# Optimization experiments

Measured on AMD Instinct MI355X. Metric: run time of the kernel, lower is better.

The kernel has to match this reference:

```python
import jax, jax.numpy as jnp
import numpy as np

B, C, H, W = 4, 64, 96, 96
O = 64          # out_channel
K = 9           # 3x3 kernel positions
PAD = 1


def conv3x3(x, w, b):
    # NCHW 3x3 conv, stride 1, pad 1
    y = jax.lax.conv_general_dilated(
        x, w, window_strides=(1, 1), padding=((PAD, PAD), (PAD, PAD)),
        dimension_numbers=("NCHW", "OIHW", "NCHW"))
    return y + b[None, :, None, None]


def deform_conv3x3(x, offset, w, b):
    """torchvision-style DeformConv2d, 3x3, stride 1, pad 1, 1 offset group.
    x: [B, Cin, H, W]; offset: [B, 2*K, H, W] ordered (dy, dx) per kernel pos.
    """
    Bb, Cin, Hh, Ww = x.shape
    off = offset.reshape(Bb, K, 2, Hh, Ww)
    ky, kx = jnp.meshgrid(jnp.arange(3), jnp.arange(3), indexing="ij")
    ky = ky.reshape(K).astype(x.dtype)
    kx = kx.reshape(K).astype(x.dtype)
    hh = jnp.arange(Hh, dtype=x.dtype)
    ww = jnp.arange(Ww, dtype=x.dtype)
    # sampling coords: p0 + p_k + delta_p  -> [B, K, H, W]
    py = hh[None, None, :, None] - PAD + ky[None, :, None, None] + off[:, :, 0]
    px = ww[None, None, None, :] - PAD + kx[None, :, None, None] + off[:, :, 1]

    y0 = jnp.floor(py).astype(jnp.int32)
    x0 = jnp.floor(px).astype(jnp.int32)
    dy = py - y0.astype(x.dtype)
    dx = px - x0.astype(x.dtype)

    x_flat = x.reshape(Bb, Cin, Hh * Ww)

    def gather(yi, xi, wgt):
        valid = ((yi >= 0) & (yi < Hh) & (xi >= 0) & (xi < Ww)).astype(x.dtype)
        idx = (jnp.clip(yi, 0, Hh - 1) * Ww + jnp.clip(xi, 0, Ww - 1)).reshape(Bb, -1)
        vals = jax.vmap(lambda xf, ix: xf[:, ix])(x_flat, idx)  # [B, Cin, K*H*W]
        return vals * (wgt * valid).reshape(Bb, 1, -1)

    sampled = (gather(y0,     x0,     (1 - dy) * (1 - dx))
             + gather(y0,     x0 + 1, (1 - dy) * dx)
             + gather(y0 + 1, x0,     dy * (1 - dx))
             + gather(y0 + 1, x0 + 1, dy * dx))
    sampled = sampled.reshape(Bb, Cin, K, Hh, Ww)
    out = jnp.einsum("bckhw,ock->bohw", sampled, w.reshape(O, Cin, K))
    return out + b[None, :, None, None]


def setup_inputs() -> dict:
    key = jax.random.key(0)
    ks = jax.random.split(key, 6)
    ref_feat = jax.random.normal(ks[0], (B, C, H, W), dtype=jnp.float32)
    dist_feat = jax.random.normal(ks[1], (B, C, H, W), dtype=jnp.float32)
    offset_w = jax.random.normal(ks[2], (2 * K, C, 3, 3), dtype=jnp.float32) * 0.01
    offset_b = jnp.zeros((2 * K,), dtype=jnp.float32)
    deform_w = jax.random.normal(ks[3], (O, 3 * C, 3, 3), dtype=jnp.float32) * 0.05
    deform_b = jax.random.normal(ks[4], (O,), dtype=jnp.float32) * 0.05
    return {"ref_feat": ref_feat, "dist_feat": dist_feat,
            "offset_w": offset_w, "offset_b": offset_b,
            "deform_w": deform_w, "deform_b": deform_b}


def reference(ref_feat, dist_feat, offset_w, offset_b, deform_w, deform_b):
    offset = conv3x3(ref_feat, offset_w, offset_b)
    diff = (ref_feat - dist_feat) ** 2
    feat_in = jnp.concatenate((ref_feat, dist_feat, diff), axis=1)  # [B, 3C, H, W]
    feat = deform_conv3x3(feat_in, offset, deform_w, deform_b)
    feat = jax.nn.relu(feat)
    return (feat, diff)
```

## Files before the change

### kernel.cpp

```cpp
#include <hip/hip_runtime.h>
#include <hip/hip_fp16.h>

#define Wd    96
#define Hd    96
#define HW    9216
#define Bn    4
#define Cn    64
#define C3    192
#define On    64
#define NPIX  (Bn*HW)
#define NFEAT (Bn*Cn*HW)
#define NWTB  (9*6*4*512)
#define NWTB2 (18*2*64*8)
#define NRB3  (Bn*(HW/32))

#define HR2   6
#define HC    21
#define HPITCH 400
#define NPR2  (HR2*HC)
#define SELEM (NPR2*24)
#define HALO_B (NPR2*HPITCH)
#define NFBLK 1152

typedef __attribute__((ext_vector_type(8))) short s8v;
typedef __attribute__((ext_vector_type(8))) _Float16 h8v;
typedef __attribute__((ext_vector_type(4))) unsigned int u4v;
typedef __attribute__((ext_vector_type(4))) float f4v;

__device__ __forceinline__ unsigned packh(float lo, float hi) {
    __half2 h = __floats2half2_rn(lo, hi);
    return __builtin_bit_cast(unsigned, h);
}

__global__ __launch_bounds__(256) void repack_wts_kernel(
        const float* __restrict__ ref,
        const float* __restrict__ dist,
        unsigned int* __restrict__ packed,
        float* __restrict__ out_diff,
        const float* __restrict__ dw,
        const float* __restrict__ ow,
        __half* __restrict__ wtb,
        __half* __restrict__ wtb2) {
    __shared__ unsigned lds[96][33];

    int tid = threadIdx.x;

    if (blockIdx.x >= NRB3) {
        int e = (int)(blockIdx.x - NRB3) * 256 + tid;
        if (e < NWTB) {
            int j = e & 7;
            int L = (e >> 3) & 63;
            int mt = (e >> 9) & 3;
            int rest = e >> 11;
            int kc = rest % 6;
            int tap = rest / 6;
            int o = mt * 16 + (L & 15);
            int c = kc * 32 + (L >> 4) * 8 + j;
            wtb[e] = __float2half(dw[((size_t)o * C3 + c) * 9 + tap]);
        } else if (e < NWTB + NWTB2) {
            int e2 = e - NWTB;
            int j = e2 & 7;
            int L = (e2 >> 3) & 63;
            int mt = (e2 >> 9) & 1;
            int kc2 = e2 >> 10;
            int v = mt * 16 + (L & 15);
            int k = kc2 * 32 + ((L >> 4) & 3) * 8 + j;
            int c = k & 63;
            int tap = k >> 6;
            float val = (v < 18) ? ow[((size_t)v * Cn + c) * 9 + tap] : 0.f;
            wtb2[e2] = __float2half(val);
        }
        return;
    }

    int blk = blockIdx.x;
    int b = blk / (HW / 32);
    int pb = (blk - b * (HW / 32)) * 32;
    int pxg = tid & 7;
    int chp = tid >> 3;

    size_t base0 = ((size_t)(b * Cn + 2 * chp)) * HW + pb + pxg * 4;
    size_t base1 = base0 + HW;

    f4v r0 = *(const f4v*)(ref + base0);
    f4v r1 = *(const f4v*)(ref + base1);
    f4v d0 = *(const f4v*)(dist + base0);
    f4v d1 = *(const f4v*)(dist + base1);

    f4v q0 = (r0 - d0) * (r0 - d0);
    f4v q1 = (r1 - d1) * (r1 - d1);
    *(f4v*)(out_diff + base0) = q0;
    *(f4v*)(out_diff + base1) = q1;

#pragma unroll
    for (int j = 0; j < 4; ++j) {
        int p = pxg * 4 + j;
        lds[chp][p]      = packh(r0[j], r1[j]);
        lds[32 + chp][p] = packh(d0[j], d1[j]);
        lds[64 + chp][p] = packh(q0[j], q1[j]);
    }
    __syncthreads();

    {
        int p = tid >> 3;
        int part = tid & 7;
        unsigned* pko = packed + ((size_t)(b * HW + pb) + p) * 96 + part * 12;
#pragma unroll
        for (int q = 0; q < 3; ++q) {
            u4v w;
#pragma unroll
            for (int j = 0; j < 4; ++j)
                w[j] = lds[part * 12 + q * 4 + j][p];
            *(u4v*)(pko + q * 4) = w;
        }
    }
}

struct Ctx {
    int o00, o01, o10, o11;
    int l00, l01, l10, l11;
    float W00, W01, W10, W11;
    int inh;
};

__device__ __forceinline__ Ctx mkctx(int t, int y, int x, int xb, int yb,
                                     float2 o2) {
    Ctx c;
    float py = (float)(y - 1 + t / 3) + o2.x;
    float pxs = (float)(x - 1 + t % 3) + o2.y;
    float fy = floorf(py), fx = floorf(pxs);
    int y0 = (int)fy, x0 = (int)fx;
    int y1 = y0 + 1, x1 = x0 + 1;
    float ay = py - fy, ax = pxs - fx;
    bool vy0 = (unsigned)y0 < (unsigned)Hd;
    bool vy1 = (unsigned)y1 < (unsigned)Hd;
    bool vx0 = (unsigned)x0 < (unsigned)Wd;
    bool vx1 = (unsigned)x1 < (unsigned)Wd;
    c.W00 = (vy0 && vx0) ? (1.f - ay) * (1.f - ax) : 0.f;
    c.W01 = (vy0 && vx1) ? (1.f - ay) * ax : 0.f;
    c.W10 = (vy1 && vx0) ? ay * (1.f - ax) : 0.f;
    c.W11 = (vy1 && vx1) ? ay * ax : 0.f;
    int y0c = min(max(y0, 0), Hd - 1), y1c = min(max(y1, 0), Hd - 1);
    int x0c = min(max(x0, 0), Wd - 1), x1c = min(max(x1, 0), Wd - 1);
    c.o00 = (y0c * Wd + x0c) * (C3 * 2);
    c.o01 = (y0c * Wd + x1c) * (C3 * 2);
    c.o10 = (y1c * Wd + x0c) * (C3 * 2);
    c.o11 = (y1c * Wd + x1c) * (C3 * 2);
    int iy0 = y0c - yb + 2, iy1 = y1c - yb + 2;
    int ix0 = x0c - xb + 3, ix1 = x1c - xb + 3;
    c.inh = ((unsigned)iy0 < (unsigned)HR2) & ((unsigned)iy1 < (unsigned)HR2) &
            ((unsigned)ix0 < (unsigned)HC) & ((unsigned)ix1 < (unsigned)HC);
    c.l00 = (iy0 * HC + ix0) * HPITCH;
    c.l01 = (iy0 * HC + ix1) * HPITCH;
    c.l10 = (iy1 * HC + ix0) * HPITCH;
    c.l11 = (iy1 * HC + ix1) * HPITCH;
    return c;
}

__device__ __forceinline__ __half2 uh2(unsigned u) {
    return __builtin_bit_cast(__half2, u);
}

__device__ __forceinline__ void bilin_mfma(const s8v* rw, const Ctx& cc,
        const s8v* __restrict__ Ap, int t, int kb, int L, f4v* acc) {
    __half2 w00 = __float2half2_rn(cc.W00);
    __half2 w01 = __float2half2_rn(cc.W01);
    __half2 w10 = __float2half2_rn(cc.W10);
    __half2 w11 = __float2half2_rn(cc.W11);
#pragma unroll
    for (int i = 0; i < 3; ++i) {
        int kc = kb + i;
        u4v u00 = __builtin_bit_cast(u4v, rw[0 * 3 + i]);
        u4v u01 = __builtin_bit_cast(u4v, rw[1 * 3 + i]);
        u4v u10 = __builtin_bit_cast(u4v, rw[2 * 3 + i]);
        u4v u11 = __builtin_bit_cast(u4v, rw[3 * 3 + i]);
        u4v bu;
#pragma unroll
        for (int p = 0; p < 4; ++p) {
            __half2 v = __hmul2(uh2(u00[p]), w00);
            v = __hfma2(uh2(u01[p]), w01, v);
            v = __hfma2(uh2(u10[p]), w10, v);
            v = __hfma2(uh2(u11[p]), w11, v);
            bu[p] = __builtin_bit_cast(unsigned, v);
        }
        h8v bfrag = __builtin_bit_cast(h8v, bu);
#pragma unroll
        for (int mt = 0; mt < 4; ++mt) {
            h8v a = __builtin_bit_cast(h8v, Ap[((t * 6 + kc) * 4 + mt) * 64 + L]);
            acc[mt] = __builtin_amdgcn_mfma_f32_16x16x32_f16(a, bfrag, acc[mt], 0, 0, 0);
        }
    }
}

__global__ __launch_bounds__(384, 4) void fused_mfma(
        const __half* __restrict__ packed,
        const __half* __restrict__ wtb2,
        const float* __restrict__ ob,
        const __half* __restrict__ wtb,
        const float* __restrict__ db,
        float* __restrict__ out) {
    __shared__ __align__(16) char smem[HALO_B + 2 * 16 * 18 * 4];
    f4v* halo = (f4v*)smem;
    float (*off_l)[18] = (float(*)[18])(smem + HALO_B);
    float* redB = (float*)smem;

    int tid = threadIdx.x;
    int L = tid & 63;
    int wv = tid >> 6;
    int g  = wv / 3;
    int kv = wv - g * 3;
    int px = L & 15;
    int lg = L >> 4;
    int blk = blockIdx.x;
    int region = (blk & 7) * 144 + (blk >> 3);
    int b = region / 288;
    int rt = region - b * 288;
    int yt = rt / 6;
    int xt = rt - yt * 6;
    int yb = yt * 2, xb = xt * 16;
    int y = yb + g, x = xb + px;
    int pb = y * Wd + xb;
    int tbase = kv * 3;

    const char* pkb = (const char*)packed + (size_t)b * HW * (C3 * 2);
    const char* hb = (const char*)halo;

    {
        f4v stg[8];
        int slot[8];
#pragma unroll
        for (int k = 0; k < 8; ++k) {
            int i = tid + k * 384;
            bool act = (k < 7) ? true : (tid < SELEM - 7 * 384);
            int pr = i / 24, ck = i - pr * 24;
            int iy = pr / HC, ix = pr - iy * HC;
            int gy = min(max(yb - 2 + iy, 0), Hd - 1);
            int gx = min(max(xb - 3 + ix, 0), Wd - 1);
            slot[k] = act ? (pr * (HPITCH / 16) + ck) : -1;
            if (act)
                stg[k] = *(const f4v*)(pkb + ((size_t)(gy * Wd + gx)) * (C3 * 2) + ck * 16);
        }
#pragma unroll
        for (int k = 0; k < 8; ++k)
            if (slot[k] >= 0) halo[slot[k]] = stg[k];
    }
    __syncthreads();

    if (kv == 0) {
        const s8v* Ap = (const s8v*)wtb2;
        f4v acc0 = {0.f, 0.f, 0.f, 0.f};
        f4v acc1 = {0.f, 0.f, 0.f, 0.f};
#pragma unroll
        for (int t = 0; t < 9; ++t) {
            int ty = t / 3, tx = t - ty * 3;
            int yy = y - 1 + ty, xx = x - 1 + tx;
            bool val = (unsigned)yy < (unsigned)Hd && (unsigned)xx < (unsigned)Wd;
            short m = val ? (short)-1 : (short)0;
            int lofs = ((g + 1 + ty) * HC + (px + 2 + tx)) * HPITCH + lg * 16;
#pragma unroll
            for (int kc = 0; kc < 2; ++kc) {
                s8v braw = *(const s8v*)(hb + lofs + kc * 64) & m;
                h8v bfrag = __builtin_bit_cast(h8v, braw);
                h8v a0 = __builtin_bit_cast(h8v, Ap[((t * 2 + kc) * 2 + 0) * 64 + L]);
                h8v a1 = __builtin_bit_cast(h8v, Ap[((t * 2 + kc) * 2 + 1) * 64 + L]);
                acc0 = __builtin_amdgcn_mfma_f32_16x16x32_f16(a0, bfrag, acc0, 0, 0, 0);
                acc1 = __builtin_amdgcn_mfma_f32_16x16x32_f16(a1, bfrag, acc1, 0, 0, 0);
            }
        }
#pragma unroll
        for (int r = 0; r < 4; ++r) {
            int v = lg * 4 + r;
            off_l[g * 16 + px][v] = acc0[r] + ob[v];
        }
        if (lg == 0) {
#pragma unroll
            for (int r = 0; r < 2; ++r)
                off_l[g * 16 + px][16 + r] = acc1[r] + ob[16 + r];
        }
    }
    __syncthreads();

    const s8v* Ap = (const s8v*)wtb;

    Ctx ctx[3];
    int ok = 1;
#pragma unroll
    for (int tt = 0; tt < 3; ++tt) {
        int t = tbase + tt;
        float2 o2 = {off_l[g * 16 + px][2 * t], off_l[g * 16 + px][2 * t + 1]};
        ctx[tt] = mkctx(t, y, x, xb, yb, o2);
        ok &= ctx[tt].inh;
    }

    f4v acc[4];
    acc[0] = acc[1] = acc[2] = acc[3] = (f4v){0.f, 0.f, 0.f, 0.f};

    if (__all(ok)) {
#pragma unroll
        for (int h = 0; h < 6; ++h) {
            int tt = h >> 1;
            int t = tbase + tt;
            int kb = (h & 1) * 3;
            const Ctx cc = ctx[tt];
            s8v rw[12];
#pragma unroll
            for (int i = 0; i < 3; ++i) {
                int co = ((kb + i) * 4 + lg) * 16;
                rw[0 * 3 + i] = *(const s8v*)(hb + cc.l00 + co);
                rw[1 * 3 + i] = *(const s8v*)(hb + cc.l01 + co);
                rw[2 * 3 + i] = *(const s8v*)(hb + cc.l10 + co);
                rw[3 * 3 + i] = *(const s8v*)(hb + cc.l11 + co);
            }
            bilin_mfma(rw, cc, Ap, t, kb, L, acc);
        }
    } else {
#pragma unroll
        for (int h = 0; h < 6; ++h) {
            int tt = h >> 1;
            int t = tbase + tt;
            int kb = (h & 1) * 3;
            const Ctx cc = ctx[tt];
            s8v rw[12];
#pragma unroll
            for (int i = 0; i < 3; ++i) {
                int co = ((kb + i) * 4 + lg) * 16;
                rw[0 * 3 + i] = *(const s8v*)(pkb + cc.o00 + co);
                rw[1 * 3 + i] = *(const s8v*)(pkb + cc.o01 + co);
                rw[2 * 3 + i] = *(const s8v*)(pkb + cc.o10 + co);
                rw[3 * 3 + i] = *(const s8v*)(pkb + cc.o11 + co);
            }
            bilin_mfma(rw, cc, Ap, t, kb, L, acc);
        }
    }

    __syncthreads();
    if (kv != 0) {
        float* r = redB + ((g * 2 + kv - 1) * 64 + L) * 17;
#pragma unroll
        for (int mt = 0; mt < 4; ++mt)
#pragma unroll
            for (int q = 0; q < 4; ++q)
                r[mt * 4 + q] = acc[mt][q];
    }
    __syncthreads();
    if (kv == 0) {
        const float* r0 = redB + ((g * 2 + 0) * 64 + L) * 17;
        const float* r1 = redB + ((g * 2 + 1) * 64 + L) * 17;
#pragma unroll
        for (int mt = 0; mt < 4; ++mt) {
#pragma unroll
            for (int q = 0; q < 4; ++q) {
                int o = mt * 16 + lg * 4 + q;
                float v = acc[mt][q] + r0[mt * 4 + q] + r1[mt * 4 + q] + db[o];
                out[((size_t)(b * On + o)) * HW + pb + px] = fmaxf(v, 0.f);
            }
        }
    }
}

extern "C" void kernel_launch(void* const* d_in, const int* in_sizes, int n_in,
                              void* d_out, int out_size, void* d_ws, size_t ws_size,
                              hipStream_t stream) {
    const float* ref  = (const float*)d_in[0];
    const float* dist = (const float*)d_in[1];
    const float* ow   = (const float*)d_in[2];
    const float* ob   = (const float*)d_in[3];
    const float* dw   = (const float*)d_in[4];
    const float* db   = (const float*)d_in[5];

    float* out = (float*)d_out;

    __half* ws_wtb  = (__half*)d_ws;
    __half* ws_wtb2 = ws_wtb + NWTB;
    __half* ws_pk   = ws_wtb2 + NWTB2;

    int wts_blocks = (NWTB + NWTB2 + 255) / 256;
    repack_wts_kernel<<<NRB3 + wts_blocks, 256, 0, stream>>>(
        ref, dist, (unsigned int*)ws_pk, out + NFEAT, dw, ow, ws_wtb, ws_wtb2);
    fused_mfma<<<NFBLK, 384, 0, stream>>>(
        ws_pk, ws_wtb2, ob, ws_wtb, db, out);
}
```

Measured before the change: 116.0 us.

## Stage halo directly into LDS with global_load_lds and XOR-swizzled layout

Replaces the register-staged halo load (global to VGPR to LDS with padded pitch 400) with direct global-to-LDS 16-byte loads. The halo is stored unpadded at 384 bytes per pixel, with each 16-byte chunk position XOR-swizzled by the pixel index to avoid LDS bank conflicts. All LDS readers (offset conv and bilinear gather) are updated to decode the swizzled address. The aim is to cut VGPR pressure and staging instructions and to shrink the LDS footprint, at the cost of extra address arithmetic on every LDS read.

After: 116.8 us. No clear change (+0.7%).

```diff
diff --git a/kernel.cpp b/kernel.cpp
--- a/kernel.cpp
+++ b/kernel.cpp
@@ -16,10 +16,10 @@
 
 #define HR2   6
 #define HC    21
-#define HPITCH 400
 #define NPR2  (HR2*HC)
 #define SELEM (NPR2*24)
-#define HALO_B (NPR2*HPITCH)
+#define HALO16 3072
+#define HALO_B (HALO16*16)
 #define NFBLK 1152
 
 typedef __attribute__((ext_vector_type(8))) short s8v;
@@ -30,6 +30,12 @@
 __device__ __forceinline__ unsigned packh(float lo, float hi) {
     __half2 h = __floats2half2_rn(lo, hi);
     return __builtin_bit_cast(unsigned, h);
+}
+
+__device__ __forceinline__ void gload_lds16(const void* g, void* l) {
+    __builtin_amdgcn_global_load_lds(
+        (const __attribute__((address_space(1))) unsigned int*)g,
+        (__attribute__((address_space(3))) unsigned int*)l, 16, 0, 0);
 }
 
 __global__ __launch_bounds__(256) void repack_wts_kernel(
@@ -150,10 +156,12 @@
     int ix0 = x0c - xb + 3, ix1 = x1c - xb + 3;
     c.inh = ((unsigned)iy0 < (unsigned)HR2) & ((unsigned)iy1 < (unsigned)HR2) &
             ((unsigned)ix0 < (unsigned)HC) & ((unsigned)ix1 < (unsigned)HC);
-    c.l00 = (iy0 * HC + ix0) * HPITCH;
-    c.l01 = (iy0 * HC + ix1) * HPITCH;
-    c.l10 = (iy1 * HC + ix0) * HPITCH;
-    c.l11 = (iy1 * HC + ix1) * HPITCH;
+    int p00 = iy0 * HC + ix0, p01 = iy0 * HC + ix1;
+    int p10 = iy1 * HC + ix0, p11 = iy1 * HC + ix1;
+    c.l00 = p00 * 384 + (p00 & 7);
+    c.l01 = p01 * 384 + (p01 & 7);
+    c.l10 = p10 * 384 + (p10 & 7);
+    c.l11 = p11 * 384 + (p11 & 7);
     return c;
 }
 
@@ -200,7 +208,6 @@
         const float* __restrict__ db,
         float* __restrict__ out) {
     __shared__ __align__(16) char smem[HALO_B + 2 * 16 * 18 * 4];
-    f4v* halo = (f4v*)smem;
     float (*off_l)[18] = (float(*)[18])(smem + HALO_B);
     float* redB = (float*)smem;
 
@@ -223,26 +230,20 @@
     int tbase = kv * 3;
 
     const char* pkb = (const char*)packed + (size_t)b * HW * (C3 * 2);
-    const char* hb = (const char*)halo;
-
-    {
-        f4v stg[8];
-        int slot[8];
-#pragma unroll
-        for (int k = 0; k < 8; ++k) {
-            int i = tid + k * 384;
-            bool act = (k < 7) ? true : (tid < SELEM - 7 * 384);
-            int pr = i / 24, ck = i - pr * 24;
-            int iy = pr / HC, ix = pr - iy * HC;
-            int gy = min(max(yb - 2 + iy, 0), Hd - 1);
-            int gx = min(max(xb - 3 + ix, 0), Wd - 1);
-            slot[k] = act ? (pr * (HPITCH / 16) + ck) : -1;
-            if (act)
-                stg[k] = *(const f4v*)(pkb + ((size_t)(gy * Wd + gx)) * (C3 * 2) + ck * 16);
-        }
-#pragma unroll
-        for (int k = 0; k < 8; ++k)
-            if (slot[k] >= 0) halo[slot[k]] = stg[k];
+    const char* hb = (const char*)smem;
+
+#pragma unroll
+    for (int s = 0; s < 8; ++s) {
+        int gi = tid + s * 384;
+        int giS = min(gi, SELEM - 1);
+        int pr = giS / 24;
+        int slot = giS - pr * 24;
+        int chblk = slot ^ (pr & 7);
+        int iy = pr / HC, ix = pr - iy * HC;
+        int gy = min(max(yb - 2 + iy, 0), Hd - 1);
+        int gx = min(max(xb - 3 + ix, 0), Wd - 1);
+        gload_lds16(pkb + ((size_t)(gy * Wd + gx)) * 384 + chblk * 16,
+                    (char*)smem + (size_t)gi * 16);
     }
     __syncthreads();
 
@@ -256,10 +257,13 @@
             int yy = y - 1 + ty, xx = x - 1 + tx;
             bool val = (unsigned)yy < (unsigned)Hd && (unsigned)xx < (unsigned)Wd;
             short m = val ? (short)-1 : (short)0;
-            int lofs = ((g + 1 + ty) * HC + (px + 2 + tx)) * HPITCH + lg * 16;
+            int pr = (g + 1 + ty) * HC + (px + 2 + tx);
+            int pbase = pr * 384;
+            int key = pr & 7;
 #pragma unroll
             for (int kc = 0; kc < 2; ++kc) {
-                s8v braw = *(const s8v*)(hb + lofs + kc * 64) & m;
+                int chblk = kc * 4 + lg;
+                s8v braw = *(const s8v*)(hb + pbase + ((chblk ^ key) << 4)) & m;
                 h8v bfrag = __builtin_bit_cast(h8v, braw);
                 h8v a0 = __builtin_bit_cast(h8v, Ap[((t * 2 + kc) * 2 + 0) * 64 + L]);
                 h8v a1 = __builtin_bit_cast(h8v, Ap[((t * 2 + kc) * 2 + 1) * 64 + L]);
@@ -302,14 +306,18 @@
             int t = tbase + tt;
             int kb = (h & 1) * 3;
             const Ctx cc = ctx[tt];
+            int b00 = cc.l00 & ~127, k00 = cc.l00 & 7;
+            int b01 = cc.l01 & ~127, k01 = cc.l01 & 7;
+            int b10 = cc.l10 & ~127, k10 = cc.l10 & 7;
+            int b11 = cc.l11 & ~127, k11 = cc.l11 & 7;
             s8v rw[12];
 #pragma unroll
             for (int i = 0; i < 3; ++i) {
-                int co = ((kb + i) * 4 + lg) * 16;
-                rw[0 * 3 + i] = *(const s8v*)(hb + cc.l00 + co);
-                rw[1 * 3 + i] = *(const s8v*)(hb + cc.l01 + co);
-                rw[2 * 3 + i] = *(const s8v*)(hb + cc.l10 + co);
-                rw[3 * 3 + i] = *(const s8v*)(hb + cc.l11 + co);
+                int cb = (kb + i) * 4 + lg;
+                rw[0 * 3 + i] = *(const s8v*)(hb + b00 + ((cb ^ k00) << 4));
+                rw[1 * 3 + i] = *(const s8v*)(hb + b01 + ((cb ^ k01) << 4));
+                rw[2 * 3 + i] = *(const s8v*)(hb + b10 + ((cb ^ k10) << 4));
+                rw[3 * 3 + i] = *(const s8v*)(hb + b11 + ((cb ^ k11) << 4));
             }
             bilin_mfma(rw, cc, Ap, t, kb, L, acc);
         }
```
